# Kernel optimization log

Measured on AMD Instinct MI355X. Metric: run time of the kernel, lower is better.

Reference implementation:

```python
import jax, jax.numpy as jnp
import numpy as np

# SLAYER neuron / simulation constants (from params)
THETA = 10.0      # spike threshold
TAU_SR = 10.0     # PSP (synaptic response) time constant
TS = 1.0          # simulation time step
TAU_RHO = 1.0     # surrogate-gradient width
SCALE_RHO = 1.0   # surrogate-gradient scale
ALPHA = float(np.exp(-TS / TAU_SR))  # leaky-filter decay per step

B, C_IN, T = 32, 156, 2048
HID, OUT = 512, 20


@jax.custom_vjp
def spike(u):
    # Hard threshold with SLAYER-style exponential surrogate gradient.
    return (u >= THETA).astype(u.dtype)

def _spike_fwd(u):
    return spike(u), u

def _spike_bwd(u, g):
    sg = (SCALE_RHO / TAU_RHO) * jnp.exp(-jnp.abs(u - THETA) / TAU_RHO)
    return (g * sg,)

spike.defvjp(_spike_fwd, _spike_bwd)


def psp(x):
    # Leaky exponential temporal filter along the LAST axis (SLAYER psp):
    # y[t] = ALPHA * y[t-1] + x[t]
    xt = jnp.moveaxis(x, -1, 0)  # [T, ...]
    def step(c, xi):
        c = ALPHA * c + xi
        return c, c
    _, y = jax.lax.scan(step, jnp.zeros_like(xt[0]), xt)
    return jnp.moveaxis(y, 0, -1)


def dense(x, W):
    # SLAYER dense layer: per-timestep fully-connected over channel dim.
    # x: [N, C, H, W, T], W: [O, C] -> [N, O, H, W, T]
    return jnp.einsum('oc,nchwt->nohwt', W, x)


def _make_perm():
    rng = np.random.default_rng(0)
    random_list = rng.permutation(np.arange(1, 40))
    perm = []
    for i in random_list:
        perm.append(2 * int(i) - 2)
        perm.append(2 * int(i) - 1)
    for i in random_list:
        perm.append(2 * int(i) - 2 + 78)
        perm.append(2 * int(i) - 1 + 78)
    return jnp.asarray(perm, dtype=jnp.int32)


def setup_inputs() -> dict:
    key = jax.random.key(0)
    k0, k1, k2, k3, k4 = jax.random.split(key, 5)
    spike_input = jax.random.randint(k0, (B, C_IN, 1, 1, T), 0, 2).astype(jnp.float32)
    W1 = jax.random.normal(k1, (HID, C_IN), dtype=jnp.float32) * (C_IN ** -0.5)
    W2 = jax.random.normal(k2, (OUT, HID), dtype=jnp.float32) * (HID ** -0.5)
    Wl1 = jax.random.normal(k3, (HID, T), dtype=jnp.float32) * (T ** -0.5)
    Wl2 = jax.random.normal(k4, (OUT, HID), dtype=jnp.float32) * (HID ** -0.5)
    perm = _make_perm()
    return {"spike_input": spike_input, "W1": W1, "W2": W2,
            "Wl1": Wl1, "Wl2": Wl2, "perm": perm}


def reference(spike_input, W1, W2, Wl1, Wl2, perm):
    # Branch 1: channel-dense over taxels, PSP + spike, twice.
    s1 = spike(psp(dense(spike_input, W1)))          # [B, HID, 1, 1, T]
    spike_output = spike(psp(dense(s1, W2)))         # [B, OUT, 1, 1, T]

    # Branch 2: transpose channel<->time, permute taxel axis, dense over time dim.
    x_t = jnp.swapaxes(spike_input, 1, 4)            # [B, T, 1, 1, C_IN]
    x_tp = x_t[..., perm]                            # gather on taxel axis
    l1 = spike(psp(dense(x_tp, Wl1)))                # [B, HID, 1, 1, C_IN]
    location_output = spike(psp(dense(l1, Wl2)))     # [B, OUT, 1, 1, C_IN]

    return jnp.concatenate([spike_output, location_output], axis=4)
```

## Files before the change

### kernel.cpp

```cpp
#include <hip/hip_runtime.h>

#define ALPHA  0.90483741803595952f
#define ALPHA8 0.44932896411722156f
#define THETA  10.0f
#define BF1    ((unsigned short)0x3F80)
#define ISCALE 0.015625f

typedef short   bf16x8 __attribute__((ext_vector_type(8)));
typedef float   f32x4  __attribute__((ext_vector_type(4)));
typedef float   f32x4v __attribute__((ext_vector_type(4)));
typedef unsigned short ushort4v __attribute__((ext_vector_type(4)));
typedef unsigned short ushort8v __attribute__((ext_vector_type(8)));
typedef unsigned char  uchar4v  __attribute__((ext_vector_type(4)));
typedef unsigned char  uchar8v  __attribute__((ext_vector_type(8)));
typedef long long i64;

#define DMA16(gsrc, ldst)                                                     \
    __builtin_amdgcn_global_load_lds(                                         \
        (const __attribute__((address_space(1))) unsigned int*)(gsrc),        \
        (__attribute__((address_space(3))) unsigned int*)(ldst), 16, 0, 0)

__device__ __forceinline__ unsigned short f2bf(float f) {
    unsigned int x = __float_as_uint(f);
    unsigned int r = (x + 0x7FFFu + ((x >> 16) & 1u)) >> 16;
    return (unsigned short)r;
}
__device__ __forceinline__ float bf2f(unsigned short h) {
    return __uint_as_float(((unsigned int)h) << 16);
}
__device__ __forceinline__ void split2(float w, unsigned short& h0,
                                       unsigned short& h1) {
    h0 = f2bf(w);          float r0 = w - bf2f(h0);
    h1 = f2bf(r0);
}
__device__ __forceinline__ unsigned char f2fp8(float f) {
    int pk = __builtin_amdgcn_cvt_pk_fp8_f32(f, 0.f, 0, false);
    return (unsigned char)(pk & 0xFF);
}
__device__ __forceinline__ float fp82f(unsigned char b) {
    return __builtin_amdgcn_cvt_f32_fp8((int)b, 0);
}

__global__ __launch_bounds__(256) void prep_scan_pack(
    const float* __restrict__ In, unsigned char* __restrict__ Infp8,
    unsigned short* __restrict__ Pbf,
    const float* __restrict__ W1,  const float* __restrict__ W2,
    const float* __restrict__ Wl1, const float* __restrict__ Wl2,
    unsigned short* __restrict__ W1p,  unsigned char* __restrict__ W2p8,
    unsigned char* __restrict__ Wl1p8, unsigned short* __restrict__ Wl2p)
{
    const int blk = blockIdx.x;
    if (blk >= 4992) {
        const int bidx = blk - 4992;
        if (bidx >= 512 && bidx < 544) {
            int m = bidx - 512;
            for (int k = threadIdx.x; k < 512; k += 256) {
                float w = (m < 20) ? W2[(long long)m * 512 + k] : 0.f;
                unsigned char h0 = f2fp8(w);
                unsigned char h1 = f2fp8(w - fp82f(h0));
                W2p8[(long long)m * 512 + k] = h0;
                W2p8[16384 + (long long)m * 512 + k] = h1;
            }
        } else if (bidx >= 544 && bidx < 1056) {
            int m = bidx - 544;
            for (int k = threadIdx.x; k < 2048; k += 256) {
                float w = Wl1[(long long)m * 2048 + k] * 64.0f;
                unsigned char h0 = f2fp8(w);
                unsigned char h1 = f2fp8(w - fp82f(h0));
                Wl1p8[(long long)m * 2048 + k] = h0;
                Wl1p8[1048576 + (long long)m * 2048 + k] = h1;
            }
        } else {
            const float* W; unsigned short* P; int M, K, Kp, Mp, m;
            if (bidx < 512) { W = W1;  P = W1p;  M = 512; K = 156; Kp = 160; Mp = 512; m = bidx; }
            else            { W = Wl2; P = Wl2p; M = 20;  K = 512; Kp = 512; Mp = 32;  m = bidx - 1056; }
            for (int k = threadIdx.x; k < Kp; k += 256) {
                float v = (m < M && k < K) ? W[(long long)m * K + k] : 0.f;
                unsigned short h0, h1;
                split2(v, h0, h1);
                P[(long long)m * Kp + k] = h0;
                P[(long long)Mp * Kp + (long long)m * Kp + k] = h1;
            }
        }
        return;
    }

    const int row = blk;
    const int tid = threadIdx.x;
    const float* x = In + (long long)row * 2048 + tid * 8;
    const unsigned char ONE8 = f2fp8(1.0f);

    float v[8];
    *(f32x4v*)&v[0] = *(const f32x4v*)x;
    *(f32x4v*)&v[4] = *(const f32x4v*)(x + 4);

    uchar8v raw;
    #pragma unroll
    for (int k = 0; k < 8; ++k) raw[k] = (v[k] >= 0.5f) ? ONE8 : (unsigned char)0;
    *(uchar8v*)(Infp8 + (long long)row * 2048 + tid * 8) = raw;

    float y = 0.f;
    #pragma unroll
    for (int k = 0; k < 8; ++k) { y = ALPHA * y + v[k]; v[k] = y; }

    __shared__ float sc[256];
    float val = y;
    sc[tid] = val;
    float m = ALPHA8;
    for (int d = 1; d < 256; d <<= 1) {
        __syncthreads();
        float p = (tid >= d) ? sc[tid - d] : 0.f;
        __syncthreads();
        val += m * p;
        sc[tid] = val;
        m *= m;
    }
    __syncthreads();
    float carry = (tid > 0) ? sc[tid - 1] : 0.f;

    ushort8v pv;
    float ak = ALPHA;
    #pragma unroll
    for (int k = 0; k < 8; ++k) {
        float yk = v[k] + ak * carry;
        ak *= ALPHA;
        pv[k] = f2bf(yk);
    }
    *(ushort8v*)(Pbf + (long long)row * 2048 + tid * 8) = pv;
}

__global__ __launch_bounds__(256) void transposeP(
    const unsigned short* __restrict__ Pbf, unsigned short* __restrict__ PT)
{
    __shared__ unsigned short Tile[64][72];
    const int t0 = blockIdx.x * 64;
    const int c0 = blockIdx.y * 64;
    const int b  = blockIdx.z;
    const int tid = threadIdx.x;

    #pragma unroll
    for (int s = 0; s < 2; ++s) {
        int id = tid + s * 256;
        int cc = id >> 3;
        int t8 = (id & 7) * 8;
        ushort8v v = {0,0,0,0,0,0,0,0};
        if (c0 + cc < 156)
            v = *(const ushort8v*)(Pbf + (long long)(b * 156 + c0 + cc) * 2048 + t0 + t8);
        *(ushort8v*)&Tile[cc][t8] = v;
    }
    __syncthreads();

    #pragma unroll
    for (int s = 0; s < 2; ++s) {
        int id = tid + s * 256;
        int t  = id >> 3;
        int c8 = (id & 7) * 8;
        if (c0 + c8 + 7 < 160) {
            unsigned short r[8];
            #pragma unroll
            for (int j = 0; j < 8; ++j) r[j] = Tile[c8 + j][t];
            *(ushort8v*)(PT + (long long)b * 327680 + (long long)(t0 + t) * 160 + c0 + c8)
                = *(ushort8v*)r;
        }
    }
}

__global__ __launch_bounds__(256) void mega_gemm1(
    const unsigned short* __restrict__ W1p,
    const unsigned short* __restrict__ PT,
    unsigned short* __restrict__ S1bits,
    const unsigned char* __restrict__ Wl1p8,
    const unsigned char* __restrict__ Infp8,
    unsigned short* __restrict__ Zp)
{
    __shared__ alignas(16) unsigned char SMEM[49152];
    const int bx  = blockIdx.x;
    const int tid = threadIdx.x;
    const int lane = tid & 63, w = tid >> 6;
    const int wy = w >> 1, wx = w & 1;
    const int l15 = lane & 15, kq = lane >> 4;
    const int key = (l15 >> 1) & 3;

    if (bx >= 1280) {
        unsigned char* Ab = SMEM;
        unsigned char* Bb = SMEM + 32768;

        const int id1 = bx - 1280;
        const int z  = id1 >> 6;
        const int m0 = ((id1 >> 4) & 3) * 128;
        const int n0 = (id1 & 15) * 128;
        const unsigned short* Tb = PT + (long long)z * 327680;

        auto dmaA = [&](int buf, int k0) {
            #pragma unroll
            for (int s = 0; s < 4; ++s) {
                int id = tid + s * 256;
                int pl = id >> 9, m = (id >> 2) & 127, g = id & 3;
                int gs = g ^ ((m >> 1) & 3);
                DMA16(W1p + (long long)pl * 81920 +
                      (long long)(m0 + m) * 160 + k0 + gs * 8,
                      Ab + buf * 16384 + id * 16);
            }
        };
        auto dmaB = [&](int buf, int k0) {
            #pragma unroll
            for (int s = 0; s < 2; ++s) {
                int id = tid + s * 256;
                int n = id >> 2, g = id & 3;
                int gs = g ^ ((n >> 1) & 3);
                DMA16(Tb + (long long)(n0 + n) * 160 + k0 + gs * 8,
                      Bb + buf * 8192 + id * 16);
            }
        };

        int aOff[2][4], bOff[4];
        #pragma unroll
        for (int pl = 0; pl < 2; ++pl)
            #pragma unroll
            for (int mt = 0; mt < 4; ++mt)
                aOff[pl][mt] = pl * 8192 + (wy * 64 + mt * 16 + l15) * 64 +
                               ((kq ^ key) * 16);
        #pragma unroll
        for (int nt = 0; nt < 4; ++nt)
            bOff[nt] = (wx * 64 + nt * 16 + l15) * 64 + ((kq ^ key) * 16);

        f32x4 acc[4][4] = {};

        dmaA(0, 0); dmaB(0, 0);
        __syncthreads();

        #pragma unroll
        for (int it = 0; it < 5; ++it) {
            const int cur = it & 1;
            if (it < 4) { dmaA(cur ^ 1, (it + 1) * 32); dmaB(cur ^ 1, (it + 1) * 32); }

            const unsigned char* Ac = Ab + cur * 16384;
            const unsigned char* Bc = Bb + cur * 8192;
            bf16x8 bfr[4];
            #pragma unroll
            for (int nt = 0; nt < 4; ++nt)
                bfr[nt] = *(const bf16x8*)(Bc + bOff[nt]);
            #pragma unroll
            for (int pl = 0; pl < 2; ++pl) {
                #pragma unroll
                for (int mt = 0; mt < 4; ++mt) {
                    bf16x8 afr = *(const bf16x8*)(Ac + aOff[pl][mt]);
                    #pragma unroll
                    for (int nt = 0; nt < 4; ++nt)
                        acc[mt][nt] = __builtin_amdgcn_mfma_f32_16x16x32_bf16(
                            afr, bfr[nt], acc[mt][nt], 0, 0, 0);
                }
            }
            __syncthreads();
        }

        unsigned short* Db = S1bits + (long long)z * 512 * 128;
        #pragma unroll
        for (int mt = 0; mt < 4; ++mt) {
            #pragma unroll
            for (int i = 0; i < 4; ++i) {
                int m = m0 + wy * 64 + mt * 16 + kq * 4 + i;
                #pragma unroll
                for (int nt = 0; nt < 4; ++nt) {
                    unsigned long long mask = __ballot(acc[mt][nt][i] >= THETA);
                    if (l15 == 0) {
                        int nchunk = (n0 + wx * 64 + nt * 16) >> 4;
                        Db[(long long)m * 128 + nchunk] =
                            (unsigned short)((mask >> (kq * 16)) & 0xFFFFu);
                    }
                }
            }
        }
    } else {
        unsigned char* Ab = SMEM;
        unsigned char* Bb = SMEM + 16384;

        const int id0 = bx;
        const int nIdx = id0 % 40;
        if (nIdx >= 39) return;
        const int rest = id0 / 40;
        const int n0  = nIdx * 128;
        const int m0  = (rest & 7) * 64;
        const int ksl = rest >> 3;
        const int ks0 = ksl * 512;

        auto dmaA8 = [&](int buf, int kk) {
            #pragma unroll
            for (int s = 0; s < 2; ++s) {
                int id = tid + s * 256;
                int pl = id >> 8, m = (id >> 2) & 63, g = id & 3;
                int gs = g ^ ((m >> 1) & 3);
                DMA16(Wl1p8 + (long long)pl * 1048576 +
                      (long long)(m0 + m) * 2048 + kk + gs * 16,
                      Ab + buf * 8192 + id * 16);
            }
        };
        auto dmaB8 = [&](int buf, int kk) {
            #pragma unroll
            for (int s = 0; s < 2; ++s) {
                int id = tid + s * 256;
                int n = id >> 2, g = id & 3;
                int gs = g ^ ((n >> 1) & 3);
                DMA16(Infp8 + (long long)(n0 + n) * 2048 + kk + gs * 16,
                      Bb + buf * 8192 + id * 16);
            }
        };

        int aO8[2][2][2], bO8[4][2];
        #pragma unroll
        for (int ks = 0; ks < 2; ++ks) {
            const int gl = ks * 2 + (kq >> 1);
            const int sub = ((gl ^ key) * 16) + (kq & 1) * 8;
            #pragma unroll
            for (int pl = 0; pl < 2; ++pl)
                #pragma unroll
                for (int mt = 0; mt < 2; ++mt)
                    aO8[pl][mt][ks] = pl * 4096 +
                        (wy * 32 + mt * 16 + l15) * 64 + sub;
            #pragma unroll
            for (int nt = 0; nt < 4; ++nt)
                bO8[nt][ks] = (wx * 64 + nt * 16 + l15) * 64 + sub;
        }

        f32x4 acc[2][4] = {};

        dmaA8(0, ks0); dmaB8(0, ks0);
        __syncthreads();

        #pragma unroll
        for (int it = 0; it < 8; ++it) {
            const int cur = it & 1;
            if (it < 7) { dmaA8(cur ^ 1, ks0 + (it + 1) * 64);
                          dmaB8(cur ^ 1, ks0 + (it + 1) * 64); }

            const unsigned char* Ac = Ab + cur * 8192;
            const unsigned char* Bc = Bb + cur * 8192;
            #pragma unroll
            for (int ks = 0; ks < 2; ++ks) {
                i64 bfr[4];
                #pragma unroll
                for (int nt = 0; nt < 4; ++nt)
                    bfr[nt] = *(const i64*)(Bc + bO8[nt][ks]);
                #pragma unroll
                for (int pl = 0; pl < 2; ++pl) {
                    #pragma unroll
                    for (int mt = 0; mt < 2; ++mt) {
                        i64 afr = *(const i64*)(Ac + aO8[pl][mt][ks]);
                        #pragma unroll
                        for (int nt = 0; nt < 4; ++nt)
                            acc[mt][nt] = __builtin_amdgcn_mfma_f32_16x16x32_fp8_fp8(
                                afr, bfr[nt], acc[mt][nt], 0, 0, 0);
                    }
                }
            }
            __syncthreads();
        }

        unsigned short* Tu = (unsigned short*)SMEM;
        #pragma unroll
        for (int mt = 0; mt < 2; ++mt) {
            #pragma unroll
            for (int i = 0; i < 4; ++i) {
                int mL = wy * 32 + mt * 16 + kq * 4 + i;
                #pragma unroll
                for (int nt = 0; nt < 4; ++nt) {
                    int nL = wx * 64 + nt * 16 + l15;
                    Tu[mL * 129 + nL] = f2bf(acc[mt][nt][i] * ISCALE);
                }
            }
        }
        __syncthreads();

        unsigned short* Zs = Zp + (long long)ksl * 2555904;
        #pragma unroll
        for (int s2 = 0; s2 < 32; ++s2) {
            int id = tid + s2 * 256;
            int cL = id >> 6;
            int mL = id & 63;
            int n = n0 + cL;
            int bb = n / 156, cc = n - bb * 156;
            Zs[(long long)cc * 16384 + bb * 512 + m0 + mL] = Tu[mL * 129 + cL];
        }
    }
}

__global__ __launch_bounds__(256) void mega_stage2(
    const unsigned char* __restrict__ W2p8,
    const unsigned short* __restrict__ S1bits,
    float* __restrict__ C2p,
    const unsigned short* __restrict__ Zp,
    const int* __restrict__ perm,
    unsigned short* __restrict__ L1T)
{
    __shared__ alignas(16) unsigned char SMEM[20608];
    const int bx  = blockIdx.x;
    const int tid = threadIdx.x;

    if (bx < 1024) {
        auto As = (unsigned char (*)[32][72])SMEM;
        auto Bs = (unsigned char (*)[72])(SMEM + 4608);

        const int lane = tid & 63, w = tid >> 6;
        const int l15 = lane & 15, kq = lane >> 4;
        const int n0  = (bx & 15) * 128;
        const int ksl = (bx >> 4) & 1;
        const int b   = bx >> 5;
        const int ks0 = ksl * 256;

        const unsigned short* Bb = S1bits + (long long)b * 512 * 128;
        const unsigned char ONE8 = f2fp8(1.0f);

        int aPl[2], aM[2], aK8[2];
        #pragma unroll
        for (int s = 0; s < 2; ++s) {
            int id = tid + s * 256;
            aPl[s] = id >> 8; int rem = id & 255;
            aM[s] = rem >> 3; aK8[s] = (rem & 7) * 8;
        }
        const int kb = (tid >> 4) * 4;
        const int nb = (tid & 15) * 8;
        const int nchunk = (n0 + nb) >> 4;
        const int nshift = nb & 15;

        f32x4 acc[2][2] = {};
        uchar8v aReg[2];
        unsigned short bBits[4];

        auto loadA = [&](int k0) {
            #pragma unroll
            for (int s = 0; s < 2; ++s)
                aReg[s] = *(const uchar8v*)(W2p8 + (long long)aPl[s] * 16384 +
                                            (long long)aM[s] * 512 + k0 + aK8[s]);
        };
        auto loadB = [&](int k0) {
            #pragma unroll
            for (int kk2 = 0; kk2 < 4; ++kk2)
                bBits[kk2] = Bb[(long long)(k0 + kb + kk2) * 128 + nchunk];
        };
        auto stage = [&]() {
            #pragma unroll
            for (int s = 0; s < 2; ++s) *(uchar8v*)&As[aPl[s]][aM[s]][aK8[s]] = aReg[s];
            unsigned char bv[4][8];
            #pragma unroll
            for (int kk2 = 0; kk2 < 4; ++kk2) {
                unsigned int bits = ((unsigned int)bBits[kk2] >> nshift) & 0xFFu;
                #pragma unroll
                for (int j = 0; j < 8; ++j)
                    bv[kk2][j] = ((bits >> j) & 1u) ? ONE8 : (unsigned char)0;
            }
            #pragma unroll
            for (int j = 0; j < 8; ++j) {
                uchar4v v4 = { bv[0][j], bv[1][j], bv[2][j], bv[3][j] };
                *(uchar4v*)&Bs[nb + j][kb] = v4;
            }
        };

        loadA(ks0); loadB(ks0);
        stage();
        __syncthreads();

        #pragma unroll
        for (int it = 0; it < 4; ++it) {
            const int kn = ks0 + (it + 1) * 64;
            if (it < 3) { loadA(kn); loadB(kn); }

            #pragma unroll
            for (int ks = 0; ks < 2; ++ks) {
                i64 bfr[2];
                #pragma unroll
                for (int nt = 0; nt < 2; ++nt)
                    bfr[nt] = *(const i64*)&Bs[w * 32 + nt * 16 + l15][ks * 32 + kq * 8];
                #pragma unroll
                for (int s = 0; s < 2; ++s) {
                    #pragma unroll
                    for (int mt = 0; mt < 2; ++mt) {
                        i64 afr = *(const i64*)&As[s][mt * 16 + l15][ks * 32 + kq * 8];
                        #pragma unroll
                        for (int nt = 0; nt < 2; ++nt)
                            acc[mt][nt] = __builtin_amdgcn_mfma_f32_16x16x32_fp8_fp8(
                                afr, bfr[nt], acc[mt][nt], 0, 0, 0);
                    }
                }
            }
            __syncthreads();
            if (it < 3) {
                stage();
                __syncthreads();
            }
        }

        float* Cb = C2p + (long long)b * 20 * 2048 + (long long)ksl * 1310720LL;
        #pragma unroll
        for (int mt = 0; mt < 2; ++mt) {
            #pragma unroll
            for (int i = 0; i < 4; ++i) {
                int m = mt * 16 + kq * 4 + i;
                if (m >= 20) continue;
                #pragma unroll
                for (int nt = 0; nt < 2; ++nt) {
                    int n = n0 + w * 32 + nt * 16 + l15;
                    Cb[(long long)m * 2048 + n] = acc[mt][nt][i];
                }
            }
        }
    } else {
        auto Xs = (float (*)[32])SMEM;
        int* p  = (int*)(SMEM + 19968);

        const int r0 = (bx - 1024) * 32;
        for (int i = tid; i < 156; i += 256) p[i] = perm[i];

        const int row = tid & 31;
        const int cq  = tid >> 5;
        #pragma unroll
        for (int it = 0; it < 20; ++it) {
            int c = it * 8 + cq;
            if (c < 156) {
                long long base = (long long)c * 16384 + r0 + row;
                float s = bf2f(Zp[base]) + bf2f(Zp[base + 2555904]) +
                          bf2f(Zp[base + 2 * 2555904]) + bf2f(Zp[base + 3 * 2555904]);
                Xs[c][row] = s;
            }
        }
        __syncthreads();

        if (tid < 32) {
            float y = 0.f;
            for (int c = 0; c < 156; ++c) {
                y = ALPHA * y + Xs[p[c]][tid];
                L1T[(long long)c * 16384 + r0 + tid] = (y >= THETA) ? BF1 : 0;
            }
        }
    }
}

__global__ __launch_bounds__(256) void mega_stage3(
    const float* __restrict__ C2p, float* __restrict__ out,
    const unsigned short* __restrict__ Wl2p,
    const unsigned short* __restrict__ L1T)
{
    __shared__ alignas(16) unsigned char SMEM[36864];
    const int bx  = blockIdx.x;
    const int tid = threadIdx.x;

    if (bx < 640) {
        float* sc = (float*)SMEM;
        const int row = bx;
        const float* x = C2p + (long long)row * 2048 + tid * 8;

        float v[8];
        #pragma unroll
        for (int k = 0; k < 8; ++k) v[k] = x[k] + x[k + 1310720LL];

        float y = 0.f;
        #pragma unroll
        for (int k = 0; k < 8; ++k) { y = ALPHA * y + v[k]; v[k] = y; }

        float val = y;
        sc[tid] = val;
        float m = ALPHA8;
        for (int d = 1; d < 256; d <<= 1) {
            __syncthreads();
            float p = (tid >= d) ? sc[tid - d] : 0.f;
            __syncthreads();
            val += m * p;
            sc[tid] = val;
            m *= m;
        }
        __syncthreads();
        float carry = (tid > 0) ? sc[tid - 1] : 0.f;

        float* o = out + (long long)row * 2204 + tid * 8;
        float ak = ALPHA;
        #pragma unroll
        for (int k = 0; k < 8; ++k) {
            float yk = v[k] + ak * carry;
            ak *= ALPHA;
            o[k] = (yk >= THETA) ? 1.0f : 0.0f;
        }
    } else {
        auto As = (unsigned short (*)[32][72])SMEM;
        auto Bs = (unsigned short (*)[72])(SMEM + 9216);

        const int b  = bx - 640;
        const int lane = tid & 63, w = tid >> 6;
        const int l15 = lane & 15, kq = lane >> 4;

        f32x4 acc[2][3] = {};

        for (int k0 = 0; k0 < 512; k0 += 64) {
            #pragma unroll
            for (int s = 0; s < 2; ++s) {
                int id = tid + s * 256;
                int pl = id >> 8, rem = id & 255;
                int m = rem >> 3, k8 = (rem & 7) * 8;
                ushort8v v = *(const ushort8v*)(Wl2p + (long long)pl * 16384 +
                                                (long long)m * 512 + k0 + k8);
                *(ushort8v*)&As[pl][m][k8] = v;
            }
            #pragma unroll
            for (int s = 0; s < 6; ++s) {
                int id = tid + s * 256;
                int n = id >> 3, k8 = (id & 7) * 8;
                ushort8v v = {0,0,0,0,0,0,0,0};
                if (n < 156)
                    v = *(const ushort8v*)(L1T + (long long)n * 16384 +
                                           b * 512 + k0 + k8);
                *(ushort8v*)&Bs[n][k8] = v;
            }
            __syncthreads();

            #pragma unroll
            for (int ks = 0; ks < 2; ++ks) {
                bf16x8 bfr[3];
                #pragma unroll
                for (int nt = 0; nt < 3; ++nt)
                    bfr[nt] = *(const bf16x8*)&Bs[w * 48 + nt * 16 + l15][ks * 32 + kq * 8];
                #pragma unroll
                for (int s = 0; s < 2; ++s) {
                    #pragma unroll
                    for (int mt = 0; mt < 2; ++mt) {
                        bf16x8 afr = *(const bf16x8*)&As[s][mt * 16 + l15][ks * 32 + kq * 8];
                        #pragma unroll
                        for (int nt = 0; nt < 3; ++nt)
                            acc[mt][nt] = __builtin_amdgcn_mfma_f32_16x16x32_bf16(
                                afr, bfr[nt], acc[mt][nt], 0, 0, 0);
                    }
                }
            }
            __syncthreads();
        }

        float* Cs = (float*)SMEM;
        #pragma unroll
        for (int mt = 0; mt < 2; ++mt) {
            #pragma unroll
            for (int i = 0; i < 4; ++i) {
                int m = mt * 16 + kq * 4 + i;
                #pragma unroll
                for (int nt = 0; nt < 3; ++nt) {
                    int n = w * 48 + nt * 16 + l15;
                    Cs[m * 193 + n] = acc[mt][nt][i];
                }
            }
        }
        __syncthreads();

        if (tid < 20) {
            const float* cr = Cs + tid * 193;
            float* o = out + (long long)(b * 20 + tid) * 2204 + 2048;
            float y = 0.f;
            for (int c = 0; c < 156; ++c) {
                y = ALPHA * y + cr[c];
                o[c] = (y >= THETA) ? 1.0f : 0.0f;
            }
        }
    }
}

extern "C" void kernel_launch(void* const* d_in, const int* in_sizes, int n_in,
                              void* d_out, int out_size, void* d_ws, size_t ws_size,
                              hipStream_t stream)
{
    const float* In  = (const float*)d_in[0];
    const float* W1  = (const float*)d_in[1];
    const float* W2  = (const float*)d_in[2];
    const float* Wl1 = (const float*)d_in[3];
    const float* Wl2 = (const float*)d_in[4];
    const int*  perm = (const int*)d_in[5];
    float* out = (float*)d_out;

    float* ws = (float*)d_ws;
    unsigned short* S1bits = (unsigned short*)ws;
    float* C2p = ws + 1048576LL;
    unsigned char*  Infp8 = (unsigned char*)(ws + 3670016LL);
    unsigned short* Pbf  = (unsigned short*)(ws + 6225920LL);
    unsigned short* PT   = (unsigned short*)(ws + 11337728LL);
    unsigned short* W1p  = (unsigned short*)(ws + 16580608LL);
    unsigned char*  W2p8 = (unsigned char*)(ws + 16662528LL);
    unsigned char*  Wl1p8= (unsigned char*)(ws + 16670720LL);
    unsigned short* Wl2p = (unsigned short*)(ws + 17195008LL);
    unsigned short* Zpbf = (unsigned short*)(ws + 17211392LL);
    unsigned short* L1T  = (unsigned short*)(ws + 22323200LL);

    dim3 blk(256);

    prep_scan_pack<<<dim3(6080), blk, 0, stream>>>(
        In, Infp8, Pbf, W1, W2, Wl1, Wl2, W1p, W2p8, Wl1p8, Wl2p);
    transposeP<<<dim3(32, 3, 32), blk, 0, stream>>>(Pbf, PT);

    mega_gemm1<<<dim3(3328), blk, 0, stream>>>(W1p, PT, S1bits,
                                               Wl1p8, Infp8, Zpbf);
    mega_stage2<<<dim3(1536), blk, 0, stream>>>(W2p8, S1bits, C2p,
                                                Zpbf, perm, L1T);
    mega_stage3<<<dim3(672), blk, 0, stream>>>(C2p, out, Wl2p, L1T);

    (void)in_sizes; (void)n_in; (void)out_size; (void)ws_size;
}
```

Baseline: 187.0 us.

## Triple-buffer B tiles with vmcnt waits and double-buffer second GEMM LDS

Both paths of mega_gemm1 now keep three B-tile LDS buffers. They replace the two __syncthreads per iteration with an explicit s_waitcnt vmcnt plus a single s_barrier, and raise wave priority around the MFMA block. The second kernel's staged A/B LDS tiles become double-buffered, so the next stage is written before one barrier instead of after two. The aim is fewer barriers and more overlap of global loads with MFMA, at the cost of more LDS per block, which may reduce occupancy. The hand-written vmcnt counts must match the number of outstanding DMA ops for correctness.

```diff
diff --git a/kernel.cpp b/kernel.cpp
--- a/kernel.cpp
+++ b/kernel.cpp
@@ -173,7 +173,7 @@
     const unsigned char* __restrict__ Infp8,
     unsigned short* __restrict__ Zp)
 {
-    __shared__ alignas(16) unsigned char SMEM[49152];
+    __shared__ alignas(16) unsigned char SMEM[57344];
     const int bx  = blockIdx.x;
     const int tid = threadIdx.x;
     const int lane = tid & 63, w = tid >> 6;
@@ -182,9 +182,6 @@
     const int key = (l15 >> 1) & 3;
 
     if (bx >= 1280) {
-        unsigned char* Ab = SMEM;
-        unsigned char* Bb = SMEM + 32768;
-
         const int id1 = bx - 1280;
         const int z  = id1 >> 6;
         const int m0 = ((id1 >> 4) & 3) * 128;
@@ -199,7 +196,7 @@
                 int gs = g ^ ((m >> 1) & 3);
                 DMA16(W1p + (long long)pl * 81920 +
                       (long long)(m0 + m) * 160 + k0 + gs * 8,
-                      Ab + buf * 16384 + id * 16);
+                      SMEM + buf * 16384 + id * 16);
             }
         };
         auto dmaB = [&](int buf, int k0) {
@@ -209,7 +206,7 @@
                 int n = id >> 2, g = id & 3;
                 int gs = g ^ ((n >> 1) & 3);
                 DMA16(Tb + (long long)(n0 + n) * 160 + k0 + gs * 8,
-                      Bb + buf * 8192 + id * 16);
+                      SMEM + 32768 + buf * 8192 + id * 16);
             }
         };
 
@@ -226,20 +223,24 @@
 
         f32x4 acc[4][4] = {};
 
-        dmaA(0, 0); dmaB(0, 0);
-        __syncthreads();
+        dmaA(0, 0); dmaB(0, 0); dmaB(1, 32);
 
         #pragma unroll
         for (int it = 0; it < 5; ++it) {
-            const int cur = it & 1;
-            if (it < 4) { dmaA(cur ^ 1, (it + 1) * 32); dmaB(cur ^ 1, (it + 1) * 32); }
-
-            const unsigned char* Ac = Ab + cur * 16384;
-            const unsigned char* Bc = Bb + cur * 8192;
+            if (it < 4) asm volatile("s_waitcnt vmcnt(2)" ::: "memory");
+            else        asm volatile("s_waitcnt vmcnt(0)" ::: "memory");
+            __builtin_amdgcn_s_barrier();
+            __builtin_amdgcn_sched_barrier(0);
+            if (it < 4) dmaA((it + 1) & 1, (it + 1) * 32);
+            if (it < 3) dmaB((it + 2) % 3, (it + 2) * 32);
+
+            const unsigned char* Ac = SMEM + (it & 1) * 16384;
+            const unsigned char* Bc = SMEM + 32768 + (it % 3) * 8192;
             bf16x8 bfr[4];
             #pragma unroll
             for (int nt = 0; nt < 4; ++nt)
                 bfr[nt] = *(const bf16x8*)(Bc + bOff[nt]);
+            __builtin_amdgcn_s_setprio(1);
             #pragma unroll
             for (int pl = 0; pl < 2; ++pl) {
                 #pragma unroll
@@ -251,7 +252,7 @@
                             afr, bfr[nt], acc[mt][nt], 0, 0, 0);
                 }
             }
-            __syncthreads();
+            __builtin_amdgcn_s_setprio(0);
         }
 
         unsigned short* Db = S1bits + (long long)z * 512 * 128;
@@ -272,9 +273,6 @@
             }
         }
     } else {
-        unsigned char* Ab = SMEM;
-        unsigned char* Bb = SMEM + 16384;
-
         const int id0 = bx;
         const int nIdx = id0 % 40;
         if (nIdx >= 39) return;
@@ -292,7 +290,7 @@
                 int gs = g ^ ((m >> 1) & 3);
                 DMA16(Wl1p8 + (long long)pl * 1048576 +
                       (long long)(m0 + m) * 2048 + kk + gs * 16,
-                      Ab + buf * 8192 + id * 16);
+                      SMEM + buf * 8192 + id * 16);
             }
         };
         auto dmaB8 = [&](int buf, int kk) {
@@ -302,7 +300,7 @@
                 int n = id >> 2, g = id & 3;
                 int gs = g ^ ((n >> 1) & 3);
                 DMA16(Infp8 + (long long)(n0 + n) * 2048 + kk + gs * 16,
-                      Bb + buf * 8192 + id * 16);
+                      SMEM + 16384 + buf * 8192 + id * 16);
             }
         };
 
@@ -324,17 +322,20 @@
 
         f32x4 acc[2][4] = {};
 
-        dmaA8(0, ks0); dmaB8(0, ks0);
-        __syncthreads();
+        dmaA8(0, ks0); dmaB8(0, ks0); dmaB8(1, ks0 + 64);
 
         #pragma unroll
         for (int it = 0; it < 8; ++it) {
-            const int cur = it & 1;
-            if (it < 7) { dmaA8(cur ^ 1, ks0 + (it + 1) * 64);
-                          dmaB8(cur ^ 1, ks0 + (it + 1) * 64); }
-
-            const unsigned char* Ac = Ab + cur * 8192;
-            const unsigned char* Bc = Bb + cur * 8192;
+            if (it < 7) asm volatile("s_waitcnt vmcnt(2)" ::: "memory");
+            else        asm volatile("s_waitcnt vmcnt(0)" ::: "memory");
+            __builtin_amdgcn_s_barrier();
+            __builtin_amdgcn_sched_barrier(0);
+            if (it < 7) dmaA8((it + 1) & 1, ks0 + (it + 1) * 64);
+            if (it < 6) dmaB8((it + 2) % 3, ks0 + (it + 2) * 64);
+
+            const unsigned char* Ac = SMEM + (it & 1) * 8192;
+            const unsigned char* Bc = SMEM + 16384 + (it % 3) * 8192;
+            __builtin_amdgcn_s_setprio(1);
             #pragma unroll
             for (int ks = 0; ks < 2; ++ks) {
                 i64 bfr[4];
@@ -353,8 +354,9 @@
                     }
                 }
             }
-            __syncthreads();
-        }
+            __builtin_amdgcn_s_setprio(0);
+        }
+        __syncthreads();
 
         unsigned short* Tu = (unsigned short*)SMEM;
         #pragma unroll
@@ -392,13 +394,13 @@
     const int* __restrict__ perm,
     unsigned short* __restrict__ L1T)
 {
-    __shared__ alignas(16) unsigned char SMEM[20608];
+    __shared__ alignas(16) unsigned char SMEM[27648];
     const int bx  = blockIdx.x;
     const int tid = threadIdx.x;
 
     if (bx < 1024) {
-        auto As = (unsigned char (*)[32][72])SMEM;
-        auto Bs = (unsigned char (*)[72])(SMEM + 4608);
+        auto As = (unsigned char (*)[2][32][72])SMEM;
+        auto Bs = (unsigned char (*)[128][72])(SMEM + 9216);
 
         const int lane = tid & 63, w = tid >> 6;
         const int l15 = lane & 15, kq = lane >> 4;
@@ -437,9 +439,9 @@
             for (int kk2 = 0; kk2 < 4; ++kk2)
                 bBits[kk2] = Bb[(long long)(k0 + kb + kk2) * 128 + nchunk];
         };
-        auto stage = [&]() {
-            #pragma unroll
-            for (int s = 0; s < 2; ++s) *(uchar8v*)&As[aPl[s]][aM[s]][aK8[s]] = aReg[s];
+        auto stage = [&](int buf) {
+            #pragma unroll
+            for (int s = 0; s < 2; ++s) *(uchar8v*)&As[buf][aPl[s]][aM[s]][aK8[s]] = aReg[s];
             unsigned char bv[4][8];
             #pragma unroll
             for (int kk2 = 0; kk2 < 4; ++kk2) {
@@ -451,16 +453,17 @@
             #pragma unroll
             for (int j = 0; j < 8; ++j) {
                 uchar4v v4 = { bv[0][j], bv[1][j], bv[2][j], bv[3][j] };
-                *(uchar4v*)&Bs[nb + j][kb] = v4;
+                *(uchar4v*)&Bs[buf][nb + j][kb] = v4;
             }
         };
 
         loadA(ks0); loadB(ks0);
-        stage();
+        stage(0);
         __syncthreads();
 
         #pragma unroll
         for (int it = 0; it < 4; ++it) {
+            const int cur = it & 1;
             const int kn = ks0 + (it + 1) * 64;
             if (it < 3) { loadA(kn); loadB(kn); }
 
@@ -469,12 +472,12 @@
                 i64 bfr[2];
                 #pragma unroll
                 for (int nt = 0; nt < 2; ++nt)
-                    bfr[nt] = *(const i64*)&Bs[w * 32 + nt * 16 + l15][ks * 32 + kq * 8];
-                #pragma unroll
-                for (int s = 0; s < 2; ++s) {
+                    bfr[nt] = *(const i64*)&Bs[cur][w * 32 + nt * 16 + l15][ks * 32 + kq * 8];
+                #pragma unroll
+                for (int pl = 0; pl < 2; ++pl) {
                     #pragma unroll
                     for (int mt = 0; mt < 2; ++mt) {
-                        i64 afr = *(const i64*)&As[s][mt * 16 + l15][ks * 32 + kq * 8];
+                        i64 afr = *(const i64*)&As[cur][pl][mt * 16 + l15][ks * 32 + kq * 8];
                         #pragma unroll
                         for (int nt = 0; nt < 2; ++nt)
                             acc[mt][nt] = __builtin_amdgcn_mfma_f32_16x16x32_fp8_fp8(
@@ -482,11 +485,9 @@
                     }
                 }
             }
+
+            if (it < 3) stage(cur ^ 1);
             __syncthreads();
-            if (it < 3) {
-                stage();
-                __syncthreads();
-            }
         }
 
         float* Cb = C2p + (long long)b * 20 * 2048 + (long long)ksl * 1310720LL;
```

Measured after the change: 192.2 us. 2.8% more time.
